# Kernel optimization log

Measured on AMD Instinct MI355X. Metric: run time of the kernel, lower is better.

The kernel has to match this reference:

```python
import jax, jax.numpy as jnp
import numpy as np


def _lsa_numpy(cost):
    """O(n^3) Jonker-Volgenant / Hungarian (shortest augmenting path with
    potentials). Returns col[i] = column assigned to row i. Matches
    scipy.optimize.linear_sum_assignment for square cost matrices."""
    n = cost.shape[0]
    u = np.zeros(n + 1)
    v = np.zeros(n + 1)
    p = np.zeros(n + 1, dtype=np.int64)   # p[j] = row matched to column j (1-based)
    way = np.zeros(n + 1, dtype=np.int64)
    for i in range(1, n + 1):
        p[0] = i
        j0 = 0
        minv = np.full(n + 1, np.inf)
        used = np.zeros(n + 1, dtype=bool)
        while True:
            used[j0] = True
            i0 = p[j0]
            free = ~used
            free[0] = False
            cur = cost[i0 - 1] - u[i0] - v[1:]
            better = free[1:] & (cur < minv[1:])
            minv[1:] = np.where(better, cur, minv[1:])
            way[1:] = np.where(better, j0, way[1:])
            masked = np.where(free[1:], minv[1:], np.inf)
            j1 = int(np.argmin(masked)) + 1
            delta = masked[j1 - 1]
            u[p[used]] += delta
            v[used] -= delta
            minv[1:] = np.where(free[1:], minv[1:] - delta, minv[1:])
            j0 = j1
            if p[j0] == 0:
                break
        while j0 != 0:
            j1 = int(way[j0])
            p[j0] = p[j1]
            j0 = j1
    col = np.zeros(n, dtype=np.int64)
    for j in range(1, n + 1):
        col[p[j] - 1] = j - 1
    return col


def _batched_lsa(costs):
    costs = np.asarray(costs, dtype=np.float64)
    return np.stack([_lsa_numpy(c) for c in costs]).astype(np.int32)


def _pairwise_dist(pred, target):
    # (B,L,1,D) - (B,1,L,D) -> L2 norm over D, matching torch.norm(x-y, dim=-1)
    return jnp.linalg.norm(pred[:, :, None, :] - target[:, None, :, :], axis=-1)


def setup_inputs() -> dict:
    key = jax.random.key(0)
    k1, k2 = jax.random.split(key)
    B, L, D = 16, 256, 128
    pred = jax.random.normal(k1, (B, L, D), dtype=jnp.float32)
    target = jax.random.normal(k2, (B, L, D), dtype=jnp.float32)
    return {"pred": pred, "target": target}


def reference(pred, target):
    B, L, _ = pred.shape
    dist = _pairwise_dist(pred, target)  # (B, L, L)
    # Hungarian assignment on the detached cost matrices (host callback, like
    # the original's .detach().cpu().numpy() + scipy linear_sum_assignment).
    cols = jax.pure_callback(
        _batched_lsa,
        jax.ShapeDtypeStruct((B, L), jnp.int32),
        jax.lax.stop_gradient(dist),
    )
    # dist[b, r, cols[b, r]] for all rows; reduction='mean' per batch, summed
    # then divided by B == global mean over all matched pairs.
    matched = jnp.take_along_axis(dist, cols[:, :, None], axis=2)[..., 0]  # (B, L)
    return jnp.mean(matched)
```

## Files before the change

### kernel.cpp

```cpp
#include <hip/hip_runtime.h>
#include <hip/hip_fp16.h>
#include <hip/hip_bf16.h>
#include <float.h>
#include <limits.h>

#define B_SZ 16
#define L_SZ 256
#define D_SZ 128

__global__ __launch_bounds__(256) void dist_kernel(const float* __restrict__ pred,
                                                   const float* __restrict__ target,
                                                   float* __restrict__ dist) {
    __shared__ float predRows[8][D_SZ];
    const int blk = blockIdx.x;
    const int b   = blk >> 5;
    const int i0  = (blk & 31) * 8;
    const int tid = threadIdx.x;

    for (int idx = tid; idx < 8 * D_SZ; idx += 256) {
        int r = idx >> 7, d = idx & (D_SZ - 1);
        predRows[r][d] = pred[((size_t)b * L_SZ + i0 + r) * D_SZ + d];
    }
    __syncthreads();

    const int j = tid;
    const float* tr = target + ((size_t)b * L_SZ + j) * D_SZ;
    float acc[8];
#pragma unroll
    for (int r = 0; r < 8; ++r) acc[r] = 0.0f;

    for (int d = 0; d < D_SZ; d += 4) {
        float4 tv = *(const float4*)(tr + d);
#pragma unroll
        for (int r = 0; r < 8; ++r) {
            float4 pv = *(const float4*)(&predRows[r][d]);
            float dx = pv.x - tv.x; acc[r] += dx * dx;
            float dy = pv.y - tv.y; acc[r] += dy * dy;
            float dz = pv.z - tv.z; acc[r] += dz * dz;
            float dw = pv.w - tv.w; acc[r] += dw * dw;
        }
    }
#pragma unroll
    for (int r = 0; r < 8; ++r)
        dist[((size_t)b * L_SZ + i0 + r) * L_SZ + j] = sqrtf(acc[r]);
}

__device__ inline int readlane_i(int x, int l) { return __builtin_amdgcn_readlane(x, l); }
__device__ inline unsigned uminu(unsigned a, unsigned b) { return a < b ? a : b; }
template <int CTRL>
__device__ inline unsigned dpp_mov(unsigned v) {
    return (unsigned)__builtin_amdgcn_update_dpp((int)v, (int)v, CTRL, 0xF, 0xF, false);
}
__device__ inline unsigned wave_umin_bcast(unsigned v) {
    unsigned a = dpp_mov<0x111>(v);
    unsigned b = dpp_mov<0x112>(v);
    v = uminu(uminu(v, a), b);
    a = dpp_mov<0x113>(v);
    b = dpp_mov<0x116>(v);
    v = uminu(uminu(v, a), b);
    a = dpp_mov<0x119>(v);
    v = uminu(v, a);
    a = dpp_mov<0x142>(v);
    v = uminu(v, a);
    a = dpp_mov<0x143>(v);
    v = uminu(v, a);
    return (unsigned)__builtin_amdgcn_readlane((int)v, 63);
}
__device__ inline void unpack4(uint2 pk, float& a, float& b, float& c, float& d) {
    union { unsigned u; __half2 h; } x, y; x.u = pk.x; y.u = pk.y;
    a = __low2float(x.h); b = __high2float(x.h);
    c = __low2float(y.h); d = __high2float(y.h);
}
#define SEL4(a0,a1,a2,a3,k) ((k)==0?(a0):(k)==1?(a1):(k)==2?(a2):(a3))

#define OFF_U      (L_SZ * L_SZ * 2)
#define OFF_CLAIM  (OFF_U + (L_SZ + 1) * 4)
#define OFF_FL     (OFF_CLAIM + (L_SZ + 1) * 4)
#define OFF_EP     (OFF_FL + (L_SZ + 1) * 4)
#define LSA_LDS_BYTES (OFF_EP + L_SZ * 4 + 4)

__global__ __launch_bounds__(64) void lsa_kernel(const float* __restrict__ dist,
                                                 double* __restrict__ partial) {
    extern __shared__ char smem[];
    float* u_lds   = (float*)(smem + OFF_U);
    int*   claimed = (int*)(smem + OFF_CLAIM);
    int*   fl      = (int*)(smem + OFF_FL);
    int*   ep      = (int*)(smem + OFF_EP);

    const int b = blockIdx.x;
    const int t = threadIdx.x;
    const float* cost = dist + (size_t)b * L_SZ * L_SZ;
    const int c0i = 4 * t, c1i = 4 * t + 1, c2i = 4 * t + 2, c3i = 4 * t + 3;

    for (int idx = t * 4; idx < L_SZ * L_SZ; idx += 256) {
        float4 f = *(const float4*)(cost + idx);
        union { unsigned u; __half2 h; } a, c;
        a.h = __floats2half2_rn(f.x, f.y);
        c.h = __floats2half2_rn(f.z, f.w);
        uint2 pk; pk.x = a.u; pk.y = c.u;
        *(uint2*)(smem + idx * 2) = pk;
    }
    __syncthreads();

    float bv0 = FLT_MAX, bv1 = FLT_MAX, bv2 = FLT_MAX, bv3 = FLT_MAX;
    int   br0 = 0, br1 = 0, br2 = 0, br3 = 0;
    for (int i = 1; i <= L_SZ; ++i) {
        uint2 cpk = *(const uint2*)(smem + (size_t)(i - 1) * (L_SZ * 2) + t * 8);
        float c0, c1, c2, c3; unpack4(cpk, c0, c1, c2, c3);
        if (c0 < bv0) { bv0 = c0; br0 = i; }
        if (c1 < bv1) { bv1 = c1; br1 = i; }
        if (c2 < bv2) { bv2 = c2; br2 = i; }
        if (c3 < bv3) { bv3 = c3; br3 = i; }
    }
    float v0 = bv0, v1 = bv1, v2 = bv2, v3 = bv3;

    for (int r = t; r <= L_SZ; r += 64) claimed[r] = INT_MAX;
    __syncthreads();
    atomicMin(&claimed[br0], c0i);
    atomicMin(&claimed[br1], c1i);
    atomicMin(&claimed[br2], c2i);
    atomicMin(&claimed[br3], c3i);
    __syncthreads();
    int p0 = (claimed[br0] == c0i) ? br0 : 0;
    int p1 = (claimed[br1] == c1i) ? br1 : 0;
    int p2 = (claimed[br2] == c2i) ? br2 : 0;
    int p3 = (claimed[br3] == c3i) ? br3 : 0;

    int nf = 0;
    for (int blk = 0; blk < 4; ++blk) {
        int r = blk * 64 + t + 1;
        bool isfree = (claimed[r] == INT_MAX);
        unsigned long long mask = __ballot(isfree);
        int before = __popcll(mask & ((1ULL << t) - 1ULL));
        if (isfree) fl[nf + before] = r;
        nf += (int)__popcll(mask);
    }
    __syncthreads();

    int numfree = nf;
    int budget = 1024;
    for (int pass = 0; pass < 2; ++pass) {
        int kq = 0, prv = numfree; numfree = 0;
        while (kq < prv && budget > 0) {
            budget--;
            int i = fl[kq]; kq++;
            uint2 cpk = *(const uint2*)(smem + (size_t)(i - 1) * (L_SZ * 2) + t * 8);
            float cc0, cc1, cc2, cc3; unpack4(cpk, cc0, cc1, cc2, cc3);
            float rc0 = cc0 - v0, rc1 = cc1 - v1, rc2 = cc2 - v2, rc3 = cc3 - v3;
            float m1 = rc0; int j1 = c0i; float m2 = FLT_MAX; int j2 = INT_MAX;
            if (rc1 < m1) { m2 = m1; j2 = j1; m1 = rc1; j1 = c1i; } else if (rc1 < m2) { m2 = rc1; j2 = c1i; }
            if (rc2 < m1) { m2 = m1; j2 = j1; m1 = rc2; j1 = c2i; } else if (rc2 < m2) { m2 = rc2; j2 = c2i; }
            if (rc3 < m1) { m2 = m1; j2 = j1; m1 = rc3; j1 = c3i; } else if (rc3 < m2) { m2 = rc3; j2 = c3i; }
#pragma unroll
            for (int off = 1; off < 64; off <<= 1) {
                float bm1 = __shfl_xor(m1, off, 64); int bj1 = __shfl_xor(j1, off, 64);
                float bm2 = __shfl_xor(m2, off, 64); int bj2 = __shfl_xor(j2, off, 64);
                bool bw = (bm1 < m1) || (bm1 == m1 && bj1 < j1);
                if (bw) {
                    if (bm2 < m1 || (bm2 == m1 && bj2 < j1)) { m2 = bm2; j2 = bj2; }
                    else { m2 = m1; j2 = j1; }
                    m1 = bm1; j1 = bj1;
                } else {
                    if (bm1 < m2 || (bm1 == m2 && bj1 < j2)) { m2 = bm1; j2 = bj1; }
                }
            }
            int t1 = j1 >> 2, k1 = j1 & 3;
            int i0 = readlane_i(SEL4(p0, p1, p2, p3, k1), t1);
            bool strict = (m1 < m2);
            int jt, i0t;
            if (strict) {
                jt = j1; i0t = i0;
                float amt = m2 - m1;
                if (t == t1) {
                    if (k1 == 0) v0 -= amt; else if (k1 == 1) v1 -= amt;
                    else if (k1 == 2) v2 -= amt; else v3 -= amt;
                }
            } else if (i0 != 0) {
                jt = j2; i0t = readlane_i(SEL4(p0, p1, p2, p3, j2 & 3), j2 >> 2);
            } else { jt = j1; i0t = 0; }
            {
                int tt = jt >> 2, kk = jt & 3;
                if (t == tt) {
                    if (kk == 0) p0 = i; else if (kk == 1) p1 = i;
                    else if (kk == 2) p2 = i; else p3 = i;
                }
            }
            if (i0t != 0) {
                if (strict) { kq--; if (t == 0) fl[kq] = i0t; }
                else        { if (t == 0) fl[numfree] = i0t; numfree++; }
            }
            __syncthreads();
        }
        if (budget <= 0) break;
    }

    __syncthreads();
    for (int r = t; r <= L_SZ; r += 64) u_lds[r] = 0.0f;
    __syncthreads();
    const __half* ch = (const __half*)smem;
    if (p0) u_lds[p0] = __half2float(ch[(size_t)(p0 - 1) * L_SZ + c0i]) - v0;
    if (p1) u_lds[p1] = __half2float(ch[(size_t)(p1 - 1) * L_SZ + c1i]) - v1;
    if (p2) u_lds[p2] = __half2float(ch[(size_t)(p2 - 1) * L_SZ + c2i]) - v2;
    if (p3) u_lds[p3] = __half2float(ch[(size_t)(p3 - 1) * L_SZ + c3i]) - v3;
    __syncthreads();

    const unsigned HB  = __float_as_uint(1e30f) & 0xFFFFFF00u;
    const unsigned hp0 = HB | (unsigned)c0i, hp1 = HB | (unsigned)c1i;
    const unsigned hp2 = HB | (unsigned)c2i, hp3 = HB | (unsigned)c3i;
    float vsh0 = v0, vsh1 = v1, vsh2 = v2, vsh3 = v3;

    for (int phase = 0; phase < 300; ++phase) {
        for (int r = t; r <= L_SZ; r += 64) claimed[r] = 0;
        __syncthreads();
        if (p0) claimed[p0] = 1;
        if (p1) claimed[p1] = 1;
        if (p2) claimed[p2] = 1;
        if (p3) claimed[p3] = 1;
        __syncthreads();
        int nfr = 0;
        for (int blk = 0; blk < 4; ++blk) {
            int r = blk * 64 + t + 1;
            bool isfree = (claimed[r] == 0);
            unsigned long long mask = __ballot(isfree);
            int before = __popcll(mask & ((1ULL << t) - 1ULL));
            if (isfree) fl[nfr + before] = r;
            nfr += (int)__popcll(mask);
        }
        __syncthreads();
        if (nfr == 0) break;

        unsigned s0 = 0x7F7FFF00u | (unsigned)c0i;
        unsigned s1 = 0x7F7FFF00u | (unsigned)c1i;
        unsigned s2 = 0x7F7FFF00u | (unsigned)c2i;
        unsigned s3 = 0x7F7FFF00u | (unsigned)c3i;
        int w0 = -1, w1 = -1, w2 = -1, w3 = -1;
        float ds0 = 0.f, ds1 = 0.f, ds2 = 0.f, ds3 = 0.f;
        int cu = 0, ru = 0;

        for (int k = 0; k < nfr; ++k) {
            int fr = fl[k];
            uint2 cr = *(const uint2*)(smem + (size_t)(fr - 1) * (L_SZ * 2) + t * 8);
            float ufr = u_lds[fr];
            float cc0, cc1, cc2, cc3; unpack4(cr, cc0, cc1, cc2, cc3);
            float n0 = fmaxf((cc0 - vsh0) - ufr, 0.0f);
            float n1 = fmaxf((cc1 - vsh1) - ufr, 0.0f);
            float n2 = fmaxf((cc2 - vsh2) - ufr, 0.0f);
            float n3 = fmaxf((cc3 - vsh3) - ufr, 0.0f);
            unsigned np0 = (__float_as_uint(n0) & 0xFFFFFF00u) | (unsigned)c0i;
            unsigned np1 = (__float_as_uint(n1) & 0xFFFFFF00u) | (unsigned)c1i;
            unsigned np2 = (__float_as_uint(n2) & 0xFFFFFF00u) | (unsigned)c2i;
            unsigned np3 = (__float_as_uint(n3) & 0xFFFFFF00u) | (unsigned)c3i;
            int src = -(fr + 1);
            bool b0 = np0 < s0, b1 = np1 < s1, b2 = np2 < s2, b3 = np3 < s3;
            w0 = b0 ? src : w0;  s0 = b0 ? np0 : s0;
            w1 = b1 ? src : w1;  s1 = b1 ? np1 : s1;
            w2 = b2 ? src : w2;  s2 = b2 ? np2 : s2;
            w3 = b3 ? src : w3;  s3 = b3 ? np3 : s3;
        }

        int found = 0;
        float dfin = 0.f;
        for (int it = 0; it < 2 * L_SZ + 4; ++it) {
            unsigned m01 = uminu(s0, s1), m23 = uminu(s2, s3);
            unsigned m4  = uminu(m01, m23);
            int kloc = (int)(m4 & 3u);
            int myi  = SEL4(p0, p1, p2, p3, kloc);

            const unsigned pk = wave_umin_bcast(m4);
            const int   j1    = (int)(pk & 255u);
            const int   t1    = j1 >> 2;
            const float delta = __uint_as_float(pk & 0xFFFFFF00u);
            const int   i1    = readlane_i(myi, t1);
            dfin = delta;

            bool e0 = (c0i == j1), e1 = (c1i == j1), e2 = (c2i == j1), e3 = (c3i == j1);
            vsh0 = e0 ? -1e30f : vsh0;  s0 = e0 ? hp0 : s0;  ds0 = e0 ? delta : ds0;
            vsh1 = e1 ? -1e30f : vsh1;  s1 = e1 ? hp1 : s1;  ds1 = e1 ? delta : ds1;
            vsh2 = e2 ? -1e30f : vsh2;  s2 = e2 ? hp2 : s2;  ds2 = e2 ? delta : ds2;
            vsh3 = e3 ? -1e30f : vsh3;  s3 = e3 ? hp3 : s3;  ds3 = e3 ? delta : ds3;

            if (i1 == 0) {
                if (t == 0) ep[found] = j1;
                found++;
                if (found == nfr) break;
                continue;
            }

            uint2 cur = *(const uint2*)(smem + (size_t)(i1 - 1) * (L_SZ * 2) + t * 8);
            float ui = u_lds[i1];
            float cc0, cc1, cc2, cc3; unpack4(cur, cc0, cc1, cc2, cc3);
            const float base = delta - ui;
            float n0 = fmaxf((cc0 - vsh0) + base, 0.0f);
            float n1 = fmaxf((cc1 - vsh1) + base, 0.0f);
            float n2 = fmaxf((cc2 - vsh2) + base, 0.0f);
            float n3 = fmaxf((cc3 - vsh3) + base, 0.0f);
            unsigned np0 = (__float_as_uint(n0) & 0xFFFFFF00u) | (unsigned)c0i;
            unsigned np1 = (__float_as_uint(n1) & 0xFFFFFF00u) | (unsigned)c1i;
            unsigned np2 = (__float_as_uint(n2) & 0xFFFFFF00u) | (unsigned)c2i;
            unsigned np3 = (__float_as_uint(n3) & 0xFFFFFF00u) | (unsigned)c3i;
            bool b0 = np0 < s0, b1 = np1 < s1, b2 = np2 < s2, b3 = np3 < s3;
            w0 = b0 ? j1 : w0;  s0 = b0 ? np0 : s0;
            w1 = b1 ? j1 : w1;  s1 = b1 ? np1 : s1;
            w2 = b2 ? j1 : w2;  s2 = b2 ? np2 : s2;
            w3 = b3 ? j1 : w3;  s3 = b3 ? np3 : s3;
        }
        __syncthreads();

        if (vsh0 < -1e29f) { u_lds[p0] += dfin - ds0; v0 += ds0 - dfin; }
        if (vsh1 < -1e29f) { u_lds[p1] += dfin - ds1; v1 += ds1 - dfin; }
        if (vsh2 < -1e29f) { u_lds[p2] += dfin - ds2; v2 += ds2 - dfin; }
        if (vsh3 < -1e29f) { u_lds[p3] += dfin - ds3; v3 += ds3 - dfin; }
        for (int k = t; k < nfr; k += 64) u_lds[fl[k]] += dfin;
        vsh0 = v0; vsh1 = v1; vsh2 = v2; vsh3 = v3;
        __syncthreads();

        for (int k = 0; k < found; ++k) {
            int je = ep[k];
            int j = je, root = -1; bool ok = true;
            for (int st = 0; st <= L_SZ; ++st) {
                int tj = j >> 2, kj = j & 3;
                int usebits = readlane_i(cu, tj);
                if ((usebits >> kj) & 1) { ok = false; break; }
                int wj = readlane_i(SEL4(w0, w1, w2, w3, kj), tj);
                if (wj < 0) {
                    root = -wj - 1;
                    int rl = (root - 1) >> 2, rb = (root - 1) & 3;
                    int rbits = readlane_i(ru, rl);
                    ok = !((rbits >> rb) & 1);
                    break;
                }
                j = wj;
            }
            if (!ok || root < 1) continue;
            j = je;
            for (int st = 0; st <= L_SZ; ++st) {
                int tj = j >> 2, kj = j & 3;
                int wj = readlane_i(SEL4(w0, w1, w2, w3, kj), tj);
                int wsafe = wj < 0 ? 0 : wj;
                int pn = (wj < 0) ? root
                        : readlane_i(SEL4(p0, p1, p2, p3, wsafe & 3), wsafe >> 2);
                if (t == tj) {
                    if (kj == 0) p0 = pn; else if (kj == 1) p1 = pn;
                    else if (kj == 2) p2 = pn; else p3 = pn;
                    cu |= (1 << kj);
                }
                if (wj < 0) break;
                j = wj;
            }
            int rl = (root - 1) >> 2, rb = (root - 1) & 3;
            if (t == rl) ru |= (1 << rb);
        }
    }

    double s = 0.0;
    s += (double)cost[(size_t)max(p0 - 1, 0) * L_SZ + c0i];
    s += (double)cost[(size_t)max(p1 - 1, 0) * L_SZ + c1i];
    s += (double)cost[(size_t)max(p2 - 1, 0) * L_SZ + c2i];
    s += (double)cost[(size_t)max(p3 - 1, 0) * L_SZ + c3i];
#pragma unroll
    for (int off = 1; off < 64; off <<= 1) s += __shfl_xor(s, off, 64);
    if (t == 0) partial[b] = s;
}

__global__ void finalize_kernel(const double* __restrict__ partial, float* __restrict__ out) {
    double s = 0.0;
    for (int b = 0; b < B_SZ; ++b) s += partial[b];
    out[0] = (float)(s / (double)(B_SZ * L_SZ));
}

extern "C" void kernel_launch(void* const* d_in, const int* in_sizes, int n_in,
                              void* d_out, int out_size, void* d_ws, size_t ws_size,
                              hipStream_t stream) {
    const float* pred   = (const float*)d_in[0];
    const float* target = (const float*)d_in[1];
    float* out = (float*)d_out;

    float*  dist    = (float*)d_ws;
    double* partial = (double*)((char*)d_ws + (size_t)B_SZ * L_SZ * L_SZ * sizeof(float));

    (void)hipFuncSetAttribute((const void*)lsa_kernel,
                              hipFuncAttributeMaxDynamicSharedMemorySize,
                              LSA_LDS_BYTES);

    dist_kernel<<<B_SZ * L_SZ / 8, 256, 0, stream>>>(pred, target, dist);
    lsa_kernel<<<B_SZ, 64, LSA_LDS_BYTES, stream>>>(dist, partial);
    finalize_kernel<<<1, 1, 0, stream>>>(partial, out);
}
```

Baseline: 2.570 ms.

## Augment one shortest path per phase and keep the free-row list in registers

Each multi-source Dijkstra phase now stops at the first free column it reaches and augments only that one path, instead of continuing until it has found as many free columns as there are free rows. This removes the per-path disjointness checks and the LDS endpoint list. The matched root is then swapped out of the free-row list, so the list is no longer rebuilt from a claimed-mask every phase. Free rows are held in four registers per lane and broadcast with readlane, which drops the per-iteration LDS reads of the list. The trade-off is that more phases may be needed, and each phase repeats the initial scan over all free rows.

After: 2.172 ms. 1.18x faster.

```diff
diff --git a/kernel.cpp b/kernel.cpp
--- a/kernel.cpp
+++ b/kernel.cpp
@@ -76,8 +76,7 @@
 #define OFF_U      (L_SZ * L_SZ * 2)
 #define OFF_CLAIM  (OFF_U + (L_SZ + 1) * 4)
 #define OFF_FL     (OFF_CLAIM + (L_SZ + 1) * 4)
-#define OFF_EP     (OFF_FL + (L_SZ + 1) * 4)
-#define LSA_LDS_BYTES (OFF_EP + L_SZ * 4 + 4)
+#define LSA_LDS_BYTES (OFF_FL + (L_SZ + 1) * 4 + 4)
 
 __global__ __launch_bounds__(64) void lsa_kernel(const float* __restrict__ dist,
                                                  double* __restrict__ partial) {
@@ -85,7 +84,6 @@
     float* u_lds   = (float*)(smem + OFF_U);
     int*   claimed = (int*)(smem + OFF_CLAIM);
     int*   fl      = (int*)(smem + OFF_FL);
-    int*   ep      = (int*)(smem + OFF_EP);
 
     const int b = blockIdx.x;
     const int t = threadIdx.x;
@@ -195,7 +193,22 @@
     }
 
     __syncthreads();
-    for (int r = t; r <= L_SZ; r += 64) u_lds[r] = 0.0f;
+    for (int r = t; r <= L_SZ; r += 64) { claimed[r] = 0; u_lds[r] = 0.0f; }
+    __syncthreads();
+    if (p0) claimed[p0] = 1;
+    if (p1) claimed[p1] = 1;
+    if (p2) claimed[p2] = 1;
+    if (p3) claimed[p3] = 1;
+    __syncthreads();
+    int nfr = 0;
+    for (int blk = 0; blk < 4; ++blk) {
+        int r = blk * 64 + t + 1;
+        bool isfree = (claimed[r] == 0);
+        unsigned long long mask = __ballot(isfree);
+        int before = __popcll(mask & ((1ULL << t) - 1ULL));
+        if (isfree) fl[nfr + before] = r;
+        nfr += (int)__popcll(mask);
+    }
     __syncthreads();
     const __half* ch = (const __half*)smem;
     if (p0) u_lds[p0] = __half2float(ch[(size_t)(p0 - 1) * L_SZ + c0i]) - v0;
@@ -209,25 +222,8 @@
     const unsigned hp2 = HB | (unsigned)c2i, hp3 = HB | (unsigned)c3i;
     float vsh0 = v0, vsh1 = v1, vsh2 = v2, vsh3 = v3;
 
-    for (int phase = 0; phase < 300; ++phase) {
-        for (int r = t; r <= L_SZ; r += 64) claimed[r] = 0;
-        __syncthreads();
-        if (p0) claimed[p0] = 1;
-        if (p1) claimed[p1] = 1;
-        if (p2) claimed[p2] = 1;
-        if (p3) claimed[p3] = 1;
-        __syncthreads();
-        int nfr = 0;
-        for (int blk = 0; blk < 4; ++blk) {
-            int r = blk * 64 + t + 1;
-            bool isfree = (claimed[r] == 0);
-            unsigned long long mask = __ballot(isfree);
-            int before = __popcll(mask & ((1ULL << t) - 1ULL));
-            if (isfree) fl[nfr + before] = r;
-            nfr += (int)__popcll(mask);
-        }
-        __syncthreads();
-        if (nfr == 0) break;
+    for (int phase = 0; phase <= L_SZ && nfr > 0; ++phase) {
+        int flr0 = fl[t], flr1 = fl[t + 64], flr2 = fl[t + 128], flr3 = fl[t + 192];
 
         unsigned s0 = 0x7F7FFF00u | (unsigned)c0i;
         unsigned s1 = 0x7F7FFF00u | (unsigned)c1i;
@@ -235,10 +231,9 @@
         unsigned s3 = 0x7F7FFF00u | (unsigned)c3i;
         int w0 = -1, w1 = -1, w2 = -1, w3 = -1;
         float ds0 = 0.f, ds1 = 0.f, ds2 = 0.f, ds3 = 0.f;
-        int cu = 0, ru = 0;
 
         for (int k = 0; k < nfr; ++k) {
-            int fr = fl[k];
+            int fr = readlane_i(SEL4(flr0, flr1, flr2, flr3, k >> 6), k & 63);
             uint2 cr = *(const uint2*)(smem + (size_t)(fr - 1) * (L_SZ * 2) + t * 8);
             float ufr = u_lds[fr];
             float cc0, cc1, cc2, cc3; unpack4(cr, cc0, cc1, cc2, cc3);
@@ -258,9 +253,8 @@
             w3 = b3 ? src : w3;  s3 = b3 ? np3 : s3;
         }
 
-        int found = 0;
-        float dfin = 0.f;
-        for (int it = 0; it < 2 * L_SZ + 4; ++it) {
+        int jS = 0; float dfin = 0.f;
+        for (int it = 0; it <= L_SZ; ++it) {
             unsigned m01 = uminu(s0, s1), m23 = uminu(s2, s3);
             unsigned m4  = uminu(m01, m23);
             int kloc = (int)(m4 & 3u);
@@ -271,20 +265,14 @@
             const int   t1    = j1 >> 2;
             const float delta = __uint_as_float(pk & 0xFFFFFF00u);
             const int   i1    = readlane_i(myi, t1);
-            dfin = delta;
+
+            if (i1 == 0 || it == L_SZ) { jS = j1; dfin = delta; break; }
 
             bool e0 = (c0i == j1), e1 = (c1i == j1), e2 = (c2i == j1), e3 = (c3i == j1);
             vsh0 = e0 ? -1e30f : vsh0;  s0 = e0 ? hp0 : s0;  ds0 = e0 ? delta : ds0;
             vsh1 = e1 ? -1e30f : vsh1;  s1 = e1 ? hp1 : s1;  ds1 = e1 ? delta : ds1;
             vsh2 = e2 ? -1e30f : vsh2;  s2 = e2 ? hp2 : s2;  ds2 = e2 ? delta : ds2;
             vsh3 = e3 ? -1e30f : vsh3;  s3 = e3 ? hp3 : s3;  ds3 = e3 ? delta : ds3;
-
-            if (i1 == 0) {
-                if (t == 0) ep[found] = j1;
-                found++;
-                if (found == nfr) break;
-                continue;
-            }
 
             uint2 cur = *(const uint2*)(smem + (size_t)(i1 - 1) * (L_SZ * 2) + t * 8);
             float ui = u_lds[i1];
@@ -304,52 +292,45 @@
             w2 = b2 ? j1 : w2;  s2 = b2 ? np2 : s2;
             w3 = b3 ? j1 : w3;  s3 = b3 ? np3 : s3;
         }
-        __syncthreads();
 
         if (vsh0 < -1e29f) { u_lds[p0] += dfin - ds0; v0 += ds0 - dfin; }
         if (vsh1 < -1e29f) { u_lds[p1] += dfin - ds1; v1 += ds1 - dfin; }
         if (vsh2 < -1e29f) { u_lds[p2] += dfin - ds2; v2 += ds2 - dfin; }
         if (vsh3 < -1e29f) { u_lds[p3] += dfin - ds3; v3 += ds3 - dfin; }
-        for (int k = t; k < nfr; k += 64) u_lds[fl[k]] += dfin;
+        if (t < nfr)      u_lds[flr0] += dfin;
+        if (t + 64 < nfr) u_lds[flr1] += dfin;
+        if (t + 128 < nfr) u_lds[flr2] += dfin;
+        if (t + 192 < nfr) u_lds[flr3] += dfin;
         vsh0 = v0; vsh1 = v1; vsh2 = v2; vsh3 = v3;
         __syncthreads();
 
-        for (int k = 0; k < found; ++k) {
-            int je = ep[k];
-            int j = je, root = -1; bool ok = true;
-            for (int st = 0; st <= L_SZ; ++st) {
-                int tj = j >> 2, kj = j & 3;
-                int usebits = readlane_i(cu, tj);
-                if ((usebits >> kj) & 1) { ok = false; break; }
-                int wj = readlane_i(SEL4(w0, w1, w2, w3, kj), tj);
-                if (wj < 0) {
-                    root = -wj - 1;
-                    int rl = (root - 1) >> 2, rb = (root - 1) & 3;
-                    int rbits = readlane_i(ru, rl);
-                    ok = !((rbits >> rb) & 1);
-                    break;
-                }
-                j = wj;
+        int root = 0;
+        int j = jS;
+        for (int st = 0; st <= L_SZ; ++st) {
+            int tj = j >> 2, kj = j & 3;
+            int wj = readlane_i(SEL4(w0, w1, w2, w3, kj), tj);
+            int wsafe = wj < 0 ? 0 : wj;
+            int pn = (wj < 0) ? (-wj - 1)
+                    : readlane_i(SEL4(p0, p1, p2, p3, wsafe & 3), wsafe >> 2);
+            if (t == tj) {
+                if (kj == 0) p0 = pn; else if (kj == 1) p1 = pn;
+                else if (kj == 2) p2 = pn; else p3 = pn;
             }
-            if (!ok || root < 1) continue;
-            j = je;
-            for (int st = 0; st <= L_SZ; ++st) {
-                int tj = j >> 2, kj = j & 3;
-                int wj = readlane_i(SEL4(w0, w1, w2, w3, kj), tj);
-                int wsafe = wj < 0 ? 0 : wj;
-                int pn = (wj < 0) ? root
-                        : readlane_i(SEL4(p0, p1, p2, p3, wsafe & 3), wsafe >> 2);
-                if (t == tj) {
-                    if (kj == 0) p0 = pn; else if (kj == 1) p1 = pn;
-                    else if (kj == 2) p2 = pn; else p3 = pn;
-                    cu |= (1 << kj);
-                }
-                if (wj < 0) break;
-                j = wj;
-            }
-            int rl = (root - 1) >> 2, rb = (root - 1) & 3;
-            if (t == rl) ru |= (1 << rb);
-        }
+            if (wj < 0) { root = -wj - 1; break; }
+            j = wj;
+        }
+
+        int idx = -1;
+#pragma unroll
+        for (int sgi = 0; sgi < 4; ++sgi) {
+            int kk = sgi * 64 + t;
+            bool hit = (kk < nfr) && (SEL4(flr0, flr1, flr2, flr3, sgi) == root);
+            unsigned long long m = __ballot(hit);
+            if (m != 0 && idx < 0) idx = sgi * 64 + (int)__ffsll((unsigned long long)m) - 1;
+        }
+        if (t == 0 && idx >= 0) fl[idx] = fl[nfr - 1];
+        nfr--;
+        __syncthreads();
     }
 
     double s = 0.0;
```
